# Kernel tuning notes

Measured on AMD Instinct MI355X. Metric: run time of the kernel, lower is better.

## Reference

```python
import jax, jax.numpy as jnp
import numpy as np

B, T, C, HS = 8, 4096, 512, 64

def setup_inputs() -> dict:
    key = jax.random.key(0)
    k1, k2, k3, k4 = jax.random.split(key, 4)
    x = jax.random.normal(k1, (B, T, C), dtype=jnp.float32)
    # causal mask (lower-triangular), int32: 1 = keep, 0 = mask out
    mask = jnp.tril(jnp.ones((T, T), dtype=jnp.int32))
    Wk = jax.random.normal(k2, (C, HS), dtype=jnp.float32) * (1.0 / np.sqrt(C))
    Wq = jax.random.normal(k3, (C, HS), dtype=jnp.float32) * (1.0 / np.sqrt(C))
    Wv = jax.random.normal(k4, (C, HS), dtype=jnp.float32) * (1.0 / np.sqrt(C))
    return {"x": x, "mask": mask, "Wk": Wk, "Wq": Wq, "Wv": Wv}

def reference(x, mask, Wk, Wq, Wv):
    # single self-attention head; scale uses C (n_embd), matching the source
    k = jnp.einsum('btc,ch->bth', x, Wk)   # [B,T,HS]
    q = jnp.einsum('btc,ch->bth', x, Wq)
    v = jnp.einsum('btc,ch->bth', x, Wv)
    scale = x.shape[-1] ** -0.5
    wei = jnp.einsum('bth,bsh->bts', q, k) * scale          # [B,T,T]
    wei = jnp.where(mask == 0, jnp.float32(-1e9), wei)
    wei = jax.nn.softmax(wei, axis=-1)
    # dropout is identity in eval mode
    out = jnp.einsum('bts,bsh->bth', wei, v)                # [B,T,HS]
    return out
```

## Files before the change

kernel.cpp:

```cpp
#include <hip/hip_runtime.h>
#include <hip/hip_bf16.h>
#include <stdint.h>

typedef unsigned short u16;
typedef __bf16 bf16x8_t __attribute__((ext_vector_type(8)));
typedef __bf16 bf16x4_t __attribute__((ext_vector_type(4)));
typedef float f32x4_t __attribute__((ext_vector_type(4)));
typedef float f32x8_t __attribute__((ext_vector_type(8)));

#define TSEQ 4096
#define CDIM 512
#define HSD  64
#define NBATCH 8

static __device__ __forceinline__ f32x4_t mfma16(bf16x8_t a, bf16x8_t b, f32x4_t c) {
  return __builtin_amdgcn_mfma_f32_16x16x32_bf16(a, b, c, 0, 0, 0);
}

static __device__ __forceinline__ u16 f2bf(float f) {
  union { __bf16 h; u16 s; } v; v.h = (__bf16)f;
  return v.s;
}
static __device__ __forceinline__ float bf2f(u16 h) {
  union { unsigned u; float f; } v; v.u = ((unsigned)h) << 16;
  return v.f;
}

static __device__ __forceinline__ bf16x8_t pack8(const float* p) {
  f32x8_t v = *(const f32x8_t*)p;
  return __builtin_convertvector(v, bf16x8_t);
}
static __device__ __forceinline__ bf16x4_t cvt4(f32x4_t v) {
  return __builtin_convertvector(v, bf16x4_t);
}

#define QSCALE (0.044194173824159216f * 1.4426950408889634f)
#define MFIX 32.0f

__global__ __launch_bounds__(256) void repack_w(const float* __restrict__ Wk,
                                                const float* __restrict__ Wq,
                                                const float* __restrict__ Wv,
                                                u16* __restrict__ pw) {
  int i = blockIdx.x * 256 + threadIdx.x;
  int j    = i & 7;
  int l15  = (i >> 3) & 15;
  int quad = (i >> 7) & 3;
  int ns   = (i >> 9) & 3;
  int kc   = (i >> 11) & 15;
  int mtx  = i >> 15;
  const float* W = (mtx == 0) ? Wk : ((mtx == 1) ? Wq : Wv);
  pw[i] = f2bf(W[(kc * 32 + quad * 8 + j) * HSD + ns * 16 + l15]);
}

__global__ __launch_bounds__(256) void proj_kernel(const float* __restrict__ x,
                                                   const u16* __restrict__ pw,
                                                   u16* __restrict__ kb,
                                                   u16* __restrict__ qb,
                                                   u16* __restrict__ vb,
                                                   u16* __restrict__ vbT,
                                                   int split) {
  const int lane = threadIdx.x & 63;
  const int wave = threadIdx.x >> 6;
  const int l15 = lane & 15, quad = lane >> 4;
  const int m = (int)blockIdx.x >> 9;
  const int rblk = (int)blockIdx.x & 511;
  const int row0 = rblk * 64 + wave * 16;

  __shared__ __align__(16) u16 VtS[64 * 72];

  const float* xr = x + (size_t)(row0 + l15) * CDIM + quad * 8;
  const u16* pwm = pw + ((size_t)m * 16 * 4 * 4 * 16) * 8;

  f32x4_t acc[4];
#pragma unroll
  for (int n = 0; n < 4; ++n) acc[n] = f32x4_t{0.f, 0.f, 0.f, 0.f};

#pragma unroll 4
  for (int kc = 0; kc < 16; ++kc) {
    bf16x8_t a0 = pack8(xr + kc * 32);
#pragma unroll
    for (int n = 0; n < 4; ++n) {
      bf16x8_t bfrag = *(const bf16x8_t*)(pwm + (size_t)(((kc * 4 + n) * 4 + quad) * 16 + l15) * 8);
      acc[n] = mfma16(a0, bfrag, acc[n]);
    }
  }

  if (m == 0) {
#pragma unroll
    for (int n = 0; n < 4; ++n) {
      const int row_base = row0 + quad * 4;
#pragma unroll
      for (int r = 0; r < 4; ++r)
        kb[(size_t)(row_base + r) * HSD + n * 16 + l15] = f2bf(acc[n][r]);
    }
  } else if (m == 1) {
#pragma unroll
    for (int n = 0; n < 4; ++n) {
      const int row_base = row0 + quad * 4;
#pragma unroll
      for (int r = 0; r < 4; ++r)
        qb[(size_t)(row_base + r) * HSD + n * 16 + l15] = f2bf(acc[n][r] * QSCALE);
    }
  } else if (!split) {
#pragma unroll
    for (int n = 0; n < 4; ++n) {
      const int row_base = row0 + quad * 4;
#pragma unroll
      for (int r = 0; r < 4; ++r)
        vb[(size_t)(row_base + r) * HSD + n * 16 + l15] = f2bf(acc[n][r]);
    }
  } else {
#pragma unroll
    for (int n = 0; n < 4; ++n) {
      int h = n * 16 + l15;
      int tl = wave * 16 + quad * 4;
      *(bf16x4_t*)&VtS[h * 72 + tl] = cvt4(acc[n]);
    }
    __syncthreads();
    const int bb = (rblk * 64) >> 12;
    const int t0 = (rblk * 64) & 4095;
#pragma unroll
    for (int it = 0; it < 2; ++it) {
      int g = it * 256 + threadIdx.x;
      int h = g >> 3;
      int cc = g & 7;
      bf16x8_t vv = *(const bf16x8_t*)&VtS[h * 72 + cc * 8];
      *(bf16x8_t*)&vbT[(size_t)(bb * HSD + h) * TSEQ + t0 + cc * 8] = vv;
    }
  }
}

__global__ __launch_bounds__(256, 3) void attn_part(const u16* __restrict__ qb,
                                                    const u16* __restrict__ kb,
                                                    const u16* __restrict__ vbT,
                                                    u16* __restrict__ pO,
                                                    float* __restrict__ pl) {
  const int e = 287 - (int)blockIdx.x;
  int g = 0;
  while (g < 7 && 4 * (g + 1) * (g + 2) <= e) ++g;
  int local = e - 4 * g * (g + 1);
  int qtl = 0;
  while (local >= g + 1) { local -= g + 1; ++qtl; }
  const int qt = 8 * g + qtl;
  const int c  = local;

  const int b = blockIdx.y;
  const int tid = threadIdx.x;
  const int lane = tid & 63;
  const int wave = tid >> 6;
  const int l15 = lane & 15, quad = lane >> 4;

  __shared__ __align__(16) u16 Ks[128 * 72];
  __shared__ __align__(16) u16 Vt[64 * 136];
  __shared__ __align__(16) u16 Ps[4][16 * 72];

  const size_t bo = (size_t)b * TSEQ * HSD;
  const u16* qp = qb + bo;
  const u16* kp = kb + bo;
  const u16* vtp = vbT + (size_t)b * HSD * TSEQ;

  const int qglob = qt * 64 + wave * 16 + l15;
  bf16x8_t qf0 = *(const bf16x8_t*)(qp + (size_t)qglob * HSD + quad * 8);
  bf16x8_t qf1 = *(const bf16x8_t*)(qp + (size_t)qglob * HSD + 32 + quad * 8);

  f32x4_t o[4];
#pragma unroll
  for (int n = 0; n < 4; ++n) o[n] = f32x4_t{0.f, 0.f, 0.f, 0.f};
  float lsum = 0.f;

  const int st_lo = c * 8;
  const int nt = min(qt - st_lo + 1, 8);
  const int npair = (nt + 1) >> 1;

  const int kr = tid >> 3;
  const int kc8 = (tid & 7) * 8;
  const int vr = tid >> 4;
  const int vc8 = (tid & 15) * 8;

  u16* myP = Ps[wave];

  const f32x4_t sinit = f32x4_t{-MFIX, -MFIX, -MFIX, -MFIX};

  bf16x8_t kst[4], vst[4];
  {
    const int s64 = st_lo * 64;
#pragma unroll
    for (int p = 0; p < 4; ++p) {
      kst[p] = *(const bf16x8_t*)(kp + (size_t)(s64 + kr + 32 * p) * HSD + kc8);
      vst[p] = *(const bf16x8_t*)(vtp + (size_t)(vr + 16 * p) * TSEQ + s64 + vc8);
    }
  }

  for (int ip = 0; ip < npair; ++ip) {
    __syncthreads();
#pragma unroll
    for (int p = 0; p < 4; ++p) {
      *(bf16x8_t*)&Ks[(kr + 32 * p) * 72 + kc8] = kst[p];
      *(bf16x8_t*)&Vt[(vr + 16 * p) * 136 + vc8] = vst[p];
    }
    if (ip + 1 < npair) {
      const int s64 = (st_lo + 2 * (ip + 1)) * 64;
#pragma unroll
      for (int p = 0; p < 4; ++p) {
        kst[p] = *(const bf16x8_t*)(kp + (size_t)(s64 + kr + 32 * p) * HSD + kc8);
        vst[p] = *(const bf16x8_t*)(vtp + (size_t)(vr + 16 * p) * TSEQ + s64 + vc8);
      }
    }
    __syncthreads();

    const int st0 = st_lo + 2 * ip;
    const int nsub = (2 * ip + 1 < nt) ? 2 : 1;
#pragma unroll 2
    for (int hs = 0; hs < nsub; ++hs) {
      const int stx = st0 + hs;
      const int roff = hs * 64;

      f32x4_t s[4];
#pragma unroll
      for (int n = 0; n < 4; ++n) {
        bf16x8_t a0 = *(const bf16x8_t*)&Ks[(roff + n * 16 + l15) * 72 + quad * 8];
        bf16x8_t a1 = *(const bf16x8_t*)&Ks[(roff + n * 16 + l15) * 72 + 32 + quad * 8];
        f32x4_t a = sinit;
        a = mfma16(a0, qf0, a);
        a = mfma16(a1, qf1, a);
        s[n] = a;
      }

      if (stx == qt) {
#pragma unroll
        for (int n = 0; n < 4; ++n) {
          int sg = stx * 64 + n * 16 + quad * 4;
#pragma unroll
          for (int r = 0; r < 4; ++r)
            if (sg + r > qglob) s[n][r] = -1e9f;
        }
      }

#pragma unroll
      for (int n = 0; n < 4; ++n) {
        f32x4_t pv;
        pv[0] = exp2f(s[n][0]);
        pv[1] = exp2f(s[n][1]);
        pv[2] = exp2f(s[n][2]);
        pv[3] = exp2f(s[n][3]);
        lsum += (pv[0] + pv[1]) + (pv[2] + pv[3]);
        *(bf16x4_t*)&myP[l15 * 72 + n * 16 + quad * 4] = cvt4(pv);
      }

      asm volatile("s_waitcnt lgkmcnt(0)" ::: "memory");

#pragma unroll
      for (int kc = 0; kc < 2; ++kc) {
        bf16x8_t pf = *(const bf16x8_t*)&myP[l15 * 72 + kc * 32 + quad * 8];
#pragma unroll
        for (int n = 0; n < 4; ++n) {
          bf16x8_t vf = *(const bf16x8_t*)&Vt[(n * 16 + l15) * 136 + roff + kc * 32 + quad * 8];
          o[n] = mfma16(pf, vf, o[n]);
        }
      }
    }
  }

  lsum += __shfl_xor(lsum, 16);
  lsum += __shfl_xor(lsum, 32);

  const int pidx = (b * 64 + qt) * 8 + c;
  u16* po = pO + (size_t)pidx * 4096;
  float* pm = pl + (size_t)pidx * 64;
#pragma unroll
  for (int n = 0; n < 4; ++n)
#pragma unroll
    for (int r = 0; r < 4; ++r)
      po[(wave * 16 + quad * 4 + r) * 64 + n * 16 + l15] = f2bf(o[n][r]);
  if (lane < 16) pm[wave * 16 + lane] = lsum;
}

__global__ __launch_bounds__(256) void attn_combine(const u16* __restrict__ pO,
                                                    const float* __restrict__ pl,
                                                    float* __restrict__ out) {
  const int tid = threadIdx.x;
  const int h2 = tid & 31;
  const int rr = tid >> 5;
  const int rowg = blockIdx.x * 8 + rr;
  const int b = rowg >> 12;
  const int t = rowg & 4095;
  const int qt = t >> 6;
  const int tr = t & 63;
  const int nc = (qt >> 3) + 1;
  const int pbase = (b * 64 + qt) * 8;

  const unsigned* pO32 = (const unsigned*)pO;
  float o0 = 0.f, o1 = 0.f, lsum = 0.f;
  for (int cc = 0; cc < nc; ++cc) {
    lsum += pl[(size_t)(pbase + cc) * 64 + tr];
    unsigned u = pO32[(size_t)(pbase + cc) * 2048 + tr * 32 + h2];
    o0 += bf2f((u16)(u & 0xffffu));
    o1 += bf2f((u16)(u >> 16));
  }
  float2 res;
  res.x = o0 / lsum;
  res.y = o1 / lsum;
  *(float2*)&out[(size_t)rowg * HSD + h2 * 2] = res;
}

__global__ __launch_bounds__(256) void attn_single(const u16* __restrict__ qb,
                                                   const u16* __restrict__ kb,
                                                   const u16* __restrict__ vb,
                                                   float* __restrict__ out) {
  const int qt = (int)gridDim.x - 1 - (int)blockIdx.x;
  const int b = blockIdx.y;
  const int lane = threadIdx.x & 63;
  const int wave = threadIdx.x >> 6;
  const int l15 = lane & 15, quad = lane >> 4;

  __shared__ __align__(16) u16 Ks[64 * 72];
  __shared__ __align__(16) u16 Vt[64 * 72];
  __shared__ __align__(16) u16 Ps[4][16 * 72];

  const size_t bo = (size_t)b * TSEQ * HSD;
  const u16* qp = qb + bo;
  const u16* kp = kb + bo;
  const u16* vp = vb + bo;

  const int qrow0 = qt * 64 + wave * 16;
  bf16x8_t qf0 = *(const bf16x8_t*)(qp + (size_t)(qrow0 + l15) * HSD + quad * 8);
  bf16x8_t qf1 = *(const bf16x8_t*)(qp + (size_t)(qrow0 + l15) * HSD + 32 + quad * 8);

  f32x4_t o[4];
#pragma unroll
  for (int n = 0; n < 4; ++n) o[n] = f32x4_t{0.f, 0.f, 0.f, 0.f};
  float lrow[4] = {0.f, 0.f, 0.f, 0.f};

  const int ldr = threadIdx.x >> 3;
  const int ldc = (threadIdx.x & 7) * 8;

  const f32x4_t sinit = f32x4_t{-MFIX, -MFIX, -MFIX, -MFIX};

  for (int st = 0; st <= qt; ++st) {
    const int s0 = st * 64;
#pragma unroll
    for (int pp = 0; pp < 2; ++pp) {
      int r = ldr + pp * 32;
      bf16x8_t kv = *(const bf16x8_t*)(kp + (size_t)(s0 + r) * HSD + ldc);
      *(bf16x8_t*)&Ks[r * 72 + ldc] = kv;
      bf16x8_t vv = *(const bf16x8_t*)(vp + (size_t)(s0 + r) * HSD + ldc);
      const u16* vu = (const u16*)&vv;
#pragma unroll
      for (int j = 0; j < 8; ++j) Vt[(ldc + j) * 72 + r] = vu[j];
    }
    __syncthreads();

    f32x4_t s[4];
#pragma unroll
    for (int n = 0; n < 4; ++n) {
      bf16x8_t k0 = *(const bf16x8_t*)&Ks[(n * 16 + l15) * 72 + quad * 8];
      bf16x8_t k1 = *(const bf16x8_t*)&Ks[(n * 16 + l15) * 72 + 32 + quad * 8];
      f32x4_t a = sinit;
      a = mfma16(qf0, k0, a);
      a = mfma16(qf1, k1, a);
      s[n] = a;
    }

    if (st == qt) {
#pragma unroll
      for (int n = 0; n < 4; ++n) {
        int sg = s0 + n * 16 + l15;
#pragma unroll
        for (int r = 0; r < 4; ++r) {
          int tg = qrow0 + quad * 4 + r;
          if (sg > tg) s[n][r] = -1e9f;
        }
      }
    }

#pragma unroll
    for (int n = 0; n < 4; ++n)
#pragma unroll
      for (int r = 0; r < 4; ++r) {
        float p = exp2f(s[n][r]);
        s[n][r] = p;
        lrow[r] += p;
      }

    u16* myP = Ps[wave];
#pragma unroll
    for (int n = 0; n < 4; ++n)
#pragma unroll
      for (int r = 0; r < 4; ++r)
        myP[(quad * 4 + r) * 72 + n * 16 + l15] = f2bf(s[n][r]);

    __syncthreads();

#pragma unroll
    for (int kc = 0; kc < 2; ++kc) {
      bf16x8_t pf = *(const bf16x8_t*)&myP[l15 * 72 + kc * 32 + quad * 8];
#pragma unroll
      for (int n = 0; n < 4; ++n) {
        bf16x8_t vf = *(const bf16x8_t*)&Vt[(n * 16 + l15) * 72 + kc * 32 + quad * 8];
        o[n] = mfma16(pf, vf, o[n]);
      }
    }
    __syncthreads();
  }

#pragma unroll
  for (int r = 0; r < 4; ++r) {
    float l = lrow[r];
    l += __shfl_xor(l, 1);
    l += __shfl_xor(l, 2);
    l += __shfl_xor(l, 4);
    l += __shfl_xor(l, 8);
    lrow[r] = l;
  }

#pragma unroll
  for (int n = 0; n < 4; ++n)
#pragma unroll
    for (int r = 0; r < 4; ++r)
      out[bo + (size_t)(qrow0 + quad * 4 + r) * HSD + n * 16 + l15] = o[n][r] / lrow[r];
}

extern "C" void kernel_launch(void* const* d_in, const int* in_sizes, int n_in,
                              void* d_out, int out_size, void* d_ws, size_t ws_size,
                              hipStream_t stream) {
  const float* x  = (const float*)d_in[0];
  const float* Wk = (const float*)d_in[2];
  const float* Wq = (const float*)d_in[3];
  const float* Wv = (const float*)d_in[4];
  float* out = (float*)d_out;

  char* base = (char*)d_ws;
  const size_t KV = (size_t)NBATCH * TSEQ * HSD;
  u16* pw  = (u16*)base;
  u16* kb  = (u16*)(base + (1 << 18));
  u16* qb  = kb + KV;
  u16* vbT = qb + KV;
  u16* pO  = vbT + KV;
  u16* vb  = pO;
  float* pl = (float*)(pO + (size_t)4096 * 4096);
  const size_t need = (size_t)(1 << 18) + 3 * KV * 2
                    + (size_t)4096 * 4096 * 2
                    + (size_t)4096 * 64 * 4;
  const int split = (ws_size >= need) ? 1 : 0;

  hipLaunchKernelGGL(repack_w, dim3(384), dim3(256), 0, stream, Wk, Wq, Wv, pw);
  hipLaunchKernelGGL(proj_kernel, dim3(1536), dim3(256), 0, stream, x, pw, kb, qb, vb, vbT, split);
  if (split) {
    hipLaunchKernelGGL(attn_part, dim3(288, NBATCH), dim3(256), 0, stream, qb, kb, vbT, pO, pl);
    hipLaunchKernelGGL(attn_combine, dim3(4096), dim3(256), 0, stream, pO, pl, out);
  } else {
    hipLaunchKernelGGL(attn_single, dim3(64, NBATCH), dim3(256), 0, stream, qb, kb, vb, out);
  }
}
```

Baseline: 215.3 us.

## Fuse K/Q/V projections per row block with LDS triple-buffered async loads

The projection kernel now computes K, Q and V together in a single block per 64-row tile, so x is read once instead of three times. It stages x and the repacked weights through LDS with global_load_lds async copies in a three-slot pipeline. The weight repack layout is reordered so all twelve N-fragments for a k-chunk are contiguous. The cost is more accumulators and 60KB of LDS per block, which lowers occupancy, and a grid of a third the size.

```diff
diff --git a/kernel.cpp b/kernel.cpp
--- a/kernel.cpp
+++ b/kernel.cpp
@@ -25,13 +25,18 @@
   union { unsigned u; float f; } v; v.u = ((unsigned)h) << 16;
   return v.f;
 }
-
 static __device__ __forceinline__ bf16x8_t pack8(const float* p) {
   f32x8_t v = *(const f32x8_t*)p;
   return __builtin_convertvector(v, bf16x8_t);
 }
 static __device__ __forceinline__ bf16x4_t cvt4(f32x4_t v) {
   return __builtin_convertvector(v, bf16x4_t);
+}
+
+static __device__ __forceinline__ void gload16(const void* g, void* l) {
+  __builtin_amdgcn_global_load_lds(
+      (const __attribute__((address_space(1))) unsigned int*)g,
+      (__attribute__((address_space(3))) unsigned int*)l, 16, 0, 0);
 }
 
 #define QSCALE (0.044194173824159216f * 1.4426950408889634f)
@@ -45,83 +50,111 @@
   int j    = i & 7;
   int l15  = (i >> 3) & 15;
   int quad = (i >> 7) & 3;
-  int ns   = (i >> 9) & 3;
-  int kc   = (i >> 11) & 15;
-  int mtx  = i >> 15;
-  const float* W = (mtx == 0) ? Wk : ((mtx == 1) ? Wq : Wv);
-  pw[i] = f2bf(W[(kc * 32 + quad * 8 + j) * HSD + ns * 16 + l15]);
-}
-
-__global__ __launch_bounds__(256) void proj_kernel(const float* __restrict__ x,
-                                                   const u16* __restrict__ pw,
-                                                   u16* __restrict__ kb,
-                                                   u16* __restrict__ qb,
-                                                   u16* __restrict__ vb,
-                                                   u16* __restrict__ vbT,
-                                                   int split) {
-  const int lane = threadIdx.x & 63;
-  const int wave = threadIdx.x >> 6;
+  int f    = i >> 9;
+  int kc   = f / 12;
+  int n12  = f - kc * 12;
+  int m    = n12 >> 2;
+  int n    = n12 & 3;
+  const float* W = (m == 0) ? Wk : ((m == 1) ? Wq : Wv);
+  pw[i] = f2bf(W[(kc * 32 + quad * 8 + j) * HSD + n * 16 + l15]);
+}
+
+__global__ __launch_bounds__(256, 2) void proj_kernel(const float* __restrict__ x,
+                                                      const u16* __restrict__ pw,
+                                                      u16* __restrict__ kb,
+                                                      u16* __restrict__ qb,
+                                                      u16* __restrict__ vb,
+                                                      u16* __restrict__ vbT,
+                                                      int split) {
+  const int tid = threadIdx.x;
+  const int lane = tid & 63;
+  const int wave = tid >> 6;
   const int l15 = lane & 15, quad = lane >> 4;
-  const int m = (int)blockIdx.x >> 9;
-  const int rblk = (int)blockIdx.x & 511;
-  const int row0 = rblk * 64 + wave * 16;
-
-  __shared__ __align__(16) u16 VtS[64 * 72];
-
-  const float* xr = x + (size_t)(row0 + l15) * CDIM + quad * 8;
-  const u16* pwm = pw + ((size_t)m * 16 * 4 * 4 * 16) * 8;
-
-  f32x4_t acc[4];
-#pragma unroll
-  for (int n = 0; n < 4; ++n) acc[n] = f32x4_t{0.f, 0.f, 0.f, 0.f};
-
-#pragma unroll 4
+  const int rblk = (int)blockIdx.x;
+  const int rowLocal = wave * 16 + l15;
+
+  __shared__ __align__(16) char SMEM[61440];
+  float (*XS)[2048] = (float (*)[2048])SMEM;
+  u16   (*PS)[6144] = (u16 (*)[6144])(SMEM + 24576);
+  u16* VtS = (u16*)SMEM;
+
+  const float* xg = x + (size_t)rblk * 64 * CDIM;
+
+  const int xrow = tid >> 3;
+  const int xch  = tid & 7;
+
+  f32x4_t acc[12];
+#pragma unroll
+  for (int n = 0; n < 12; ++n) acc[n] = f32x4_t{0.f, 0.f, 0.f, 0.f};
+
+  auto STAGE = [&](int slot, int kc) {
+#pragma unroll
+    for (int p = 0; p < 2; ++p) {
+      const float* src = xg + (size_t)(p * 32 + xrow) * CDIM + kc * 32 + xch * 4;
+      gload16(src, (char*)&XS[slot][0] + p * 4096 + tid * 16);
+    }
+#pragma unroll
+    for (int r = 0; r < 3; ++r) {
+      int f = r * 256 + tid;
+      gload16(pw + (size_t)kc * 6144 + (size_t)f * 8, (char*)&PS[slot][0] + f * 16);
+    }
+  };
+
+  STAGE(0, 0);
+  STAGE(1, 1);
+
+  int slot = 0;
   for (int kc = 0; kc < 16; ++kc) {
-    bf16x8_t a0 = pack8(xr + kc * 32);
-#pragma unroll
-    for (int n = 0; n < 4; ++n) {
-      bf16x8_t bfrag = *(const bf16x8_t*)(pwm + (size_t)(((kc * 4 + n) * 4 + quad) * 16 + l15) * 8);
-      acc[n] = mfma16(a0, bfrag, acc[n]);
-    }
-  }
-
-  if (m == 0) {
-#pragma unroll
-    for (int n = 0; n < 4; ++n) {
-      const int row_base = row0 + quad * 4;
+    if (kc < 15) asm volatile("s_waitcnt vmcnt(5)" ::: "memory");
+    else         asm volatile("s_waitcnt vmcnt(0)" ::: "memory");
+    __builtin_amdgcn_s_barrier();
+
+    if (kc + 2 < 16) {
+      int s2 = slot + 2; if (s2 >= 3) s2 -= 3;
+      STAGE(s2, kc + 2);
+    }
+
+    f32x8_t xv = *(const f32x8_t*)&XS[slot][rowLocal * 32 + quad * 8];
+    bf16x8_t a = __builtin_convertvector(xv, bf16x8_t);
+#pragma unroll
+    for (int n12 = 0; n12 < 12; ++n12) {
+      bf16x8_t b = *(const bf16x8_t*)&PS[slot][((n12 * 4 + quad) * 16 + l15) * 8];
+      acc[n12] = mfma16(a, b, acc[n12]);
+    }
+
+    ++slot; if (slot >= 3) slot = 0;
+  }
+
+  const int row_base = rblk * 64 + wave * 16 + quad * 4;
+#pragma unroll
+  for (int n = 0; n < 4; ++n) {
+#pragma unroll
+    for (int r = 0; r < 4; ++r) {
+      kb[(size_t)(row_base + r) * HSD + n * 16 + l15] = f2bf(acc[n][r]);
+      qb[(size_t)(row_base + r) * HSD + n * 16 + l15] = f2bf(acc[4 + n][r] * QSCALE);
+    }
+  }
+
+  if (!split) {
+#pragma unroll
+    for (int n = 0; n < 4; ++n)
 #pragma unroll
       for (int r = 0; r < 4; ++r)
-        kb[(size_t)(row_base + r) * HSD + n * 16 + l15] = f2bf(acc[n][r]);
-    }
-  } else if (m == 1) {
-#pragma unroll
-    for (int n = 0; n < 4; ++n) {
-      const int row_base = row0 + quad * 4;
-#pragma unroll
-      for (int r = 0; r < 4; ++r)
-        qb[(size_t)(row_base + r) * HSD + n * 16 + l15] = f2bf(acc[n][r] * QSCALE);
-    }
-  } else if (!split) {
-#pragma unroll
-    for (int n = 0; n < 4; ++n) {
-      const int row_base = row0 + quad * 4;
-#pragma unroll
-      for (int r = 0; r < 4; ++r)
-        vb[(size_t)(row_base + r) * HSD + n * 16 + l15] = f2bf(acc[n][r]);
-    }
+        vb[(size_t)(row_base + r) * HSD + n * 16 + l15] = f2bf(acc[8 + n][r]);
   } else {
+    __syncthreads();
 #pragma unroll
     for (int n = 0; n < 4; ++n) {
       int h = n * 16 + l15;
       int tl = wave * 16 + quad * 4;
-      *(bf16x4_t*)&VtS[h * 72 + tl] = cvt4(acc[n]);
+      *(bf16x4_t*)&VtS[h * 72 + tl] = cvt4(acc[8 + n]);
     }
     __syncthreads();
     const int bb = (rblk * 64) >> 12;
     const int t0 = (rblk * 64) & 4095;
 #pragma unroll
     for (int it = 0; it < 2; ++it) {
-      int g = it * 256 + threadIdx.x;
+      int g = it * 256 + tid;
       int h = g >> 3;
       int cc = g & 7;
       bf16x8_t vv = *(const bf16x8_t*)&VtS[h * 72 + cc * 8];
@@ -444,7 +477,7 @@
   const int split = (ws_size >= need) ? 1 : 0;
 
   hipLaunchKernelGGL(repack_w, dim3(384), dim3(256), 0, stream, Wk, Wq, Wv, pw);
-  hipLaunchKernelGGL(proj_kernel, dim3(1536), dim3(256), 0, stream, x, pw, kb, qb, vb, vbT, split);
+  hipLaunchKernelGGL(proj_kernel, dim3(512), dim3(256), 0, stream, x, pw, kb, qb, vb, vbT, split);
   if (split) {
     hipLaunchKernelGGL(attn_part, dim3(288, NBATCH), dim3(256), 0, stream, qb, kb, vbT, pO, pl);
     hipLaunchKernelGGL(attn_combine, dim3(4096), dim3(256), 0, stream, pO, pl, out);
```

After: 195.9 us. 1.1x faster.
